# Kernel optimization log

Measured on AMD Instinct MI355X. Metric: run time of the kernel, lower is better.

Reference implementation:

```python
import jax, jax.numpy as jnp
import numpy as np

N = 50000       # num_node
E = 800000      # num edges (avg degree 32)
F_IN, F_HID, F_OUT = 128, 128, 64


def setup_inputs() -> dict:
    key = jax.random.key(0)
    ks = jax.random.split(key, 8)
    x = jax.random.normal(ks[0], (N, F_IN), dtype=jnp.float32)
    edge_index = jax.random.randint(ks[1], (2, E), 0, N, dtype=jnp.int64)
    edge_weight = jax.random.uniform(ks[2], (E,), dtype=jnp.float32)
    s1 = 1.0 / np.sqrt(F_IN)
    s2 = 1.0 / np.sqrt(F_HID)
    W1 = jax.random.normal(ks[3], (F_HID, F_IN), dtype=jnp.float32) * s1
    b1 = jnp.zeros((F_HID,), dtype=jnp.float32)
    W2 = jax.random.normal(ks[4], (F_HID, F_HID), dtype=jnp.float32) * s2
    b2 = jnp.zeros((F_HID,), dtype=jnp.float32)
    W3 = jax.random.normal(ks[5], (F_OUT, F_HID), dtype=jnp.float32) * s2
    b3 = jnp.zeros((F_OUT,), dtype=jnp.float32)
    return {"x": x, "edge_index": edge_index, "edge_weight": edge_weight,
            "W1": W1, "b1": b1, "W2": W2, "b2": b2, "W3": W3, "b3": b3}


def _gcn_norm(edge_index, edge_weight, num_nodes):
    # PyG gcn_norm: add self-loops (weight 1), symmetric D^-1/2 (A+I) D^-1/2
    loop = jnp.arange(num_nodes, dtype=edge_index.dtype)
    row = jnp.concatenate([edge_index[0], loop])  # source
    col = jnp.concatenate([edge_index[1], loop])  # target (aggregation index)
    ew = jnp.concatenate([edge_weight, jnp.ones((num_nodes,), edge_weight.dtype)])
    deg = jax.ops.segment_sum(ew, col, num_segments=num_nodes)
    deg_safe = jnp.where(deg > 0, deg, 1.0)
    dinv = jnp.where(deg > 0, jax.lax.rsqrt(deg_safe), 0.0)
    norm = dinv[row] * ew * dinv[col]  # [E+N]
    return row, col, norm


def reference(x, edge_index, edge_weight, W1, b1, W2, b2, W3, b3):
    num_nodes = x.shape[0]
    row, col, norm = _gcn_norm(edge_index, edge_weight, num_nodes)
    h = x
    for W, b in ((W1, b1), (W2, b2), (W3, b3)):
        m = h @ W.T                                   # [N, d_out]
        msg = m[row] * norm[:, None]                  # gather + scale, [E+N, d_out]
        agg = jax.ops.segment_sum(msg, col, num_segments=num_nodes)
        h = jax.nn.relu(agg + b)                      # GCNConv bias then ReLU
    return h.reshape(-1)                              # torch.flatten
```

## Files before the change

kernel.cpp:

```cpp
#include <hip/hip_runtime.h>
#include <hip/hip_fp16.h>


#define K_DIM 128
#define SORT_ITEMS 4096

typedef unsigned long long u64;
typedef unsigned int u32;

using half8   = __attribute__((ext_vector_type(8))) _Float16;
using floatx4 = __attribute__((ext_vector_type(4))) float;


__global__ void build_hist(const int* __restrict__ row, const int* __restrict__ col,
                           const float* __restrict__ ew, u64* __restrict__ el,
                           u32* __restrict__ ghist, int E, int N, int nb,
                           const float* __restrict__ W1, const float* __restrict__ W2,
                           const float* __restrict__ W3, __half* __restrict__ Wh,
                           int nw1, int nw2, int nw3) {
    const int b = blockIdx.x;
    if (b >= nb) {
        const int i = (b - nb) * 256 + threadIdx.x;
        const int tot = nw1 + nw2 + nw3;
        if (i < tot) {
            float v = (i < nw1) ? W1[i] : (i < nw1 + nw2 ? W2[i - nw1] : W3[i - nw1 - nw2]);
            Wh[i] = __float2half_rn(v);
        }
        return;
    }
    __shared__ u32 bin[256];
    bin[threadIdx.x] = 0;
    __syncthreads();
    const int total = E + N;
    const int base = b * SORT_ITEMS;
    const int end = min(base + SORT_ITEMS, total);
    for (int i = base + threadIdx.x; i < end; i += 256) {
        u64 e;
        if (i < E) {
            e = ((u64)(u32)col[i] << 48) | ((u64)(u32)row[i] << 32)
              | (u64)__float_as_uint(ew[i]);
        } else {
            int v = i - E;
            e = ((u64)(u32)v << 48) | ((u64)(u32)v << 32)
              | (u64)__float_as_uint(1.0f);
        }
        el[i] = e;
        atomicAdd(&bin[(u32)(e >> 56)], 1u);
    }
    __syncthreads();
    ghist[(size_t)threadIdx.x * nb + b] = bin[threadIdx.x];
}

__global__ void digit_sum(const u32* __restrict__ ghist, u32* __restrict__ dsum, int nb) {
    __shared__ u32 s[256];
    const int d = blockIdx.x;
    u32 acc = 0;
    for (int i = threadIdx.x; i < nb; i += 256) acc += ghist[(size_t)d * nb + i];
    s[threadIdx.x] = acc;
    __syncthreads();
    for (int off = 128; off > 0; off >>= 1) {
        if (threadIdx.x < off) s[threadIdx.x] += s[threadIdx.x + off];
        __syncthreads();
    }
    if (threadIdx.x == 0) dsum[d] = s[0];
}

__global__ void digit_scan(u32* __restrict__ ghist, const u32* __restrict__ dsum,
                           u32* __restrict__ dbase, int nb) {
    __shared__ u32 ds[256];
    __shared__ u32 s[256];
    const int d = blockIdx.x, t = threadIdx.x;
    ds[t] = dsum[t];
    __syncthreads();
    for (int off = 1; off < 256; off <<= 1) {
        u32 u = (t >= off) ? ds[t - off] : 0;
        __syncthreads();
        ds[t] += u;
        __syncthreads();
    }
    u32 carry = (d == 0) ? 0u : ds[d - 1];
    if (t == 0) dbase[d] = carry;
    if (d == 255 && t == 0) dbase[256] = ds[255];
    for (int base = 0; base < nb; base += 256) {
        const int i = base + t;
        const u32 v = (i < nb) ? ghist[(size_t)d * nb + i] : 0;
        s[t] = v;
        __syncthreads();
        for (int off = 1; off < 256; off <<= 1) {
            u32 u = (t >= off) ? s[t - off] : 0;
            __syncthreads();
            s[t] += u;
            __syncthreads();
        }
        if (i < nb) ghist[(size_t)d * nb + i] = carry + s[t] - v;
        carry += s[255];
        __syncthreads();
    }
}

__global__ void p1_scatter(const u64* __restrict__ el, const u32* __restrict__ ghist,
                           u64* __restrict__ out, int total, int nb) {
    __shared__ u32 cur[256];
    cur[threadIdx.x] = ghist[(size_t)threadIdx.x * nb + blockIdx.x];
    __syncthreads();
    const int base = blockIdx.x * SORT_ITEMS;
    const int end = min(base + SORT_ITEMS, total);
    for (int i = base + threadIdx.x; i < end; i += 256) {
        u64 e = el[i];
        u32 p = atomicAdd(&cur[(u32)(e >> 56)], 1u);
        out[p] = e;
    }
}

__global__ void p2_sort(const u64* __restrict__ in, u64* __restrict__ out,
                        const u32* __restrict__ dbase,
                        int* __restrict__ offs, float* __restrict__ dinv, int n) {
    const int t = threadIdx.x;
    const int base = (int)dbase[blockIdx.x];
    const int size = (int)dbase[blockIdx.x + 1] - base;
    __shared__ u32 hist[256], cur[256], s[256];
    __shared__ float wsum[256];
    hist[t] = 0;
    wsum[t] = 0.f;
    __syncthreads();
    for (int i = t; i < size; i += 256)
        atomicAdd(&hist[(u32)(in[base + i] >> 48) & 0xFFu], 1u);
    __syncthreads();
    const u32 v = hist[t];
    s[t] = v;
    __syncthreads();
    for (int off = 1; off < 256; off <<= 1) {
        u32 u = (t >= off) ? s[t - off] : 0;
        __syncthreads();
        s[t] += u;
        __syncthreads();
    }
    const u32 mystart = (u32)base + s[t] - v;
    cur[t] = mystart;
    __syncthreads();
    for (int i = t; i < size; i += 256) {
        u64 e = in[base + i];
        u32 lo = (u32)(e >> 48) & 0xFFu;
        u32 p = atomicAdd(&cur[lo], 1u);
        out[p] = e;
        atomicAdd(&wsum[lo], __uint_as_float((u32)(e & 0xFFFFFFFFu)));
    }
    __syncthreads();
    const int node = blockIdx.x * 256 + t;
    if (node < n && v > 0) {
        offs[node] = (int)mystart;
        dinv[node] = rsqrtf(wsum[t]);
        if (node == n - 1) offs[n] = (int)(mystart + v);
    }
}


template <int BN, bool FP32IN>
__global__ __launch_bounds__(256) void mfma_gemm(const void* __restrict__ Ain,
                                                 const __half* __restrict__ Wh,
                                                 const float* __restrict__ dinv,
                                                 __half* __restrict__ C, int nrows) {
    constexpr int NT = BN / 16;
    const int wave = threadIdx.x >> 6;
    const int lane = threadIdx.x & 63;
    const int quad = lane >> 4;
    const int l16  = lane & 15;
    const int row0 = blockIdx.x * 64 + wave * 16;

    int arow = row0 + l16;
    if (arow > nrows - 1) arow = nrows - 1;

    floatx4 acc[NT] = {};

#pragma unroll
    for (int kc = 0; kc < 4; ++kc) {
        const int kof = kc * 32 + quad * 8;
        half8 af;
        if constexpr (FP32IN) {
            const float* ap = (const float*)Ain + (size_t)arow * K_DIM + kof;
            float4 f0 = *(const float4*)ap;
            float4 f1 = *(const float4*)(ap + 4);
            af[0] = (_Float16)f0.x; af[1] = (_Float16)f0.y;
            af[2] = (_Float16)f0.z; af[3] = (_Float16)f0.w;
            af[4] = (_Float16)f1.x; af[5] = (_Float16)f1.y;
            af[6] = (_Float16)f1.z; af[7] = (_Float16)f1.w;
        } else {
            af = *(const half8*)((const __half*)Ain + (size_t)arow * K_DIM + kof);
        }
#pragma unroll
        for (int ct = 0; ct < NT; ++ct) {
            half8 bf = *(const half8*)(Wh + (size_t)(ct * 16 + l16) * K_DIM + kof);
            acc[ct] = __builtin_amdgcn_mfma_f32_16x16x32_f16(af, bf, acc[ct], 0, 0, 0);
        }
    }

    float dv[4];
    int grow[4];
    bool ok[4];
#pragma unroll
    for (int r = 0; r < 4; ++r) {
        grow[r] = row0 + quad * 4 + r;
        ok[r] = grow[r] < nrows;
        dv[r] = ok[r] ? dinv[grow[r]] : 0.f;
    }
#pragma unroll
    for (int ct = 0; ct < NT; ++ct) {
        const int colb = ct * 16 + l16;
#pragma unroll
        for (int r = 0; r < 4; ++r)
            if (ok[r])
                C[(size_t)grow[r] * BN + colb] = __float2half_rn(acc[ct][r] * dv[r]);
    }
}


template <int D, typename OUT>
__global__ __launch_bounds__(256) void agg_kernel(
    const __half* __restrict__ m, const int* __restrict__ offs,
    const int2* __restrict__ csr, const float* __restrict__ dinv,
    const float* __restrict__ bias, OUT* __restrict__ out, int n) {
    const int wid = threadIdx.x >> 6;
    const int lane = threadIdx.x & 63;
    const int node = (blockIdx.x << 2) + wid;
    if (node >= n) return;
    const int beg = offs[node];
    const int end = offs[node + 1];
    const __half2* mh = (const __half2*)m;
    float acc0 = 0.f, acc1 = 0.f;

    if constexpr (D == 128) {
        int k = beg;
        for (; k + 8 <= end; k += 8) {
            int2 e[8];
            float2 f[8];
#pragma unroll
            for (int j = 0; j < 8; ++j) e[j] = csr[k + j];
#pragma unroll
            for (int j = 0; j < 8; ++j)
                f[j] = __half22float2(mh[(size_t)(e[j].y & 0xFFFF) * 64 + lane]);
#pragma unroll
            for (int j = 0; j < 8; ++j) {
                float w = __int_as_float(e[j].x);
                acc0 = fmaf(w, f[j].x, acc0);
                acc1 = fmaf(w, f[j].y, acc1);
            }
        }
        for (; k < end; ++k) {
            int2 e0 = csr[k];
            float w0 = __int_as_float(e0.x);
            float2 f0 = __half22float2(mh[(size_t)(e0.y & 0xFFFF) * 64 + lane]);
            acc0 = fmaf(w0, f0.x, acc0); acc1 = fmaf(w0, f0.y, acc1);
        }
        const float dv = dinv[node];
        const float2 bv = *(const float2*)(bias + 2 * lane);
        float ox = fmaxf(acc0 * dv + bv.x, 0.f);
        float oy = fmaxf(acc1 * dv + bv.y, 0.f);
        if constexpr (sizeof(OUT) == 2) {
            ((__half2*)out)[(size_t)node * 64 + lane] = __floats2half2_rn(ox, oy);
        } else {
            *(float2*)((float*)out + (size_t)node * 128 + 2 * lane) = make_float2(ox, oy);
        }
    } else {
        const int half = lane >> 5;
        const int sl = lane & 31;
        int k = beg;
        for (; k + 8 <= end; k += 8) {
            int2 e0 = csr[k + half], e1 = csr[k + 2 + half];
            int2 e2 = csr[k + 4 + half], e3 = csr[k + 6 + half];
            float2 f0 = __half22float2(mh[(size_t)(e0.y & 0xFFFF) * 32 + sl]);
            float2 f1 = __half22float2(mh[(size_t)(e1.y & 0xFFFF) * 32 + sl]);
            float2 f2 = __half22float2(mh[(size_t)(e2.y & 0xFFFF) * 32 + sl]);
            float2 f3 = __half22float2(mh[(size_t)(e3.y & 0xFFFF) * 32 + sl]);
            float w0 = __int_as_float(e0.x), w1 = __int_as_float(e1.x);
            float w2 = __int_as_float(e2.x), w3 = __int_as_float(e3.x);
            acc0 = fmaf(w0, f0.x, acc0); acc1 = fmaf(w0, f0.y, acc1);
            acc0 = fmaf(w1, f1.x, acc0); acc1 = fmaf(w1, f1.y, acc1);
            acc0 = fmaf(w2, f2.x, acc0); acc1 = fmaf(w2, f2.y, acc1);
            acc0 = fmaf(w3, f3.x, acc0); acc1 = fmaf(w3, f3.y, acc1);
        }
        for (; k + 2 <= end; k += 2) {
            int2 e0 = csr[k + half];
            float w0 = __int_as_float(e0.x);
            float2 f0 = __half22float2(mh[(size_t)(e0.y & 0xFFFF) * 32 + sl]);
            acc0 = fmaf(w0, f0.x, acc0); acc1 = fmaf(w0, f0.y, acc1);
        }
        if (k < end && half == 0) {
            int2 e0 = csr[k];
            float w0 = __int_as_float(e0.x);
            float2 f0 = __half22float2(mh[(size_t)(e0.y & 0xFFFF) * 32 + sl]);
            acc0 = fmaf(w0, f0.x, acc0); acc1 = fmaf(w0, f0.y, acc1);
        }
        acc0 += __shfl_xor(acc0, 32);
        acc1 += __shfl_xor(acc1, 32);
        if (half == 0) {
            const float dv = dinv[node];
            const float2 bv = *(const float2*)(bias + 2 * sl);
            float ox = fmaxf(acc0 * dv + bv.x, 0.f);
            float oy = fmaxf(acc1 * dv + bv.y, 0.f);
            *(float2*)((float*)out + (size_t)node * 64 + 2 * sl) = make_float2(ox, oy);
        }
    }
}


extern "C" void kernel_launch(void* const* d_in, const int* in_sizes, int n_in,
                              void* d_out, int out_size, void* d_ws, size_t ws_size,
                              hipStream_t stream) {
    const float* x  = (const float*)d_in[0];
    const int*   ei = (const int*)d_in[1];
    const float* ew = (const float*)d_in[2];
    const float* W1 = (const float*)d_in[3];
    const float* b1 = (const float*)d_in[4];
    const float* W2 = (const float*)d_in[5];
    const float* b2 = (const float*)d_in[6];
    const float* W3 = (const float*)d_in[7];
    const float* b3 = (const float*)d_in[8];
    float* out = (float*)d_out;

    const int N = in_sizes[0] / K_DIM;
    const int E = in_sizes[2];
    const int* row = ei;
    const int* col = ei + E;

    const int total = E + N;
    const int nb = (total + SORT_ITEMS - 1) / SORT_ITEMS;
    const int ngroups = (N + 255) >> 8;
    const int NW1 = 128 * 128, NW2 = 128 * 128, NW3 = 64 * 128;
    const int nwb = (NW1 + NW2 + NW3 + 255) / 256;

    u64* elA      = (u64*)d_ws;
    u64* elB      = elA + total;
    __half* m_buf = (__half*)(elB + total);
    __half* h_buf = m_buf + (size_t)N * K_DIM;
    __half* Wh    = h_buf + (size_t)N * K_DIM;
    u32* ghist    = (u32*)(Wh + NW1 + NW2 + NW3);
    u32* dsum     = ghist + (size_t)256 * nb;
    u32* dbase    = dsum + 256;
    int* offs     = (int*)(dbase + 257);
    float* dinv   = (float*)(offs + N + 1);

    build_hist<<<nb + nwb, 256, 0, stream>>>(row, col, ew, elA, ghist, E, N, nb,
                                             W1, W2, W3, Wh, NW1, NW2, NW3);
    digit_sum<<<256, 256, 0, stream>>>(ghist, dsum, nb);
    digit_scan<<<256, 256, 0, stream>>>(ghist, dsum, dbase, nb);
    p1_scatter<<<nb, 256, 0, stream>>>(elA, ghist, elB, total, nb);
    p2_sort<<<ngroups, 256, 0, stream>>>(elB, elA, dbase, offs, dinv, N);

    const int gemm_blocks = (N + 63) / 64;
    const int agg_blocks = (N + 3) / 4;
    const int2* csr = (const int2*)elA;

    mfma_gemm<128, true><<<gemm_blocks, 256, 0, stream>>>(x, Wh, dinv, m_buf, N);
    agg_kernel<128, __half><<<agg_blocks, 256, 0, stream>>>(m_buf, offs, csr, dinv, b1, h_buf, N);
    mfma_gemm<128, false><<<gemm_blocks, 256, 0, stream>>>(h_buf, Wh + NW1, dinv, m_buf, N);
    agg_kernel<128, __half><<<agg_blocks, 256, 0, stream>>>(m_buf, offs, csr, dinv, b2, h_buf, N);
    mfma_gemm<64, false><<<gemm_blocks, 256, 0, stream>>>(h_buf, Wh + NW1 + NW2, dinv, m_buf, N);
    agg_kernel<64, float><<<agg_blocks, 256, 0, stream>>>(m_buf, offs, csr, dinv, b3, out, N);
}
```

Baseline: 303.5 us.

## Fuse aggregation with next-layer GEMM and trim sort kernel launches

```diff
diff --git a/kernel.cpp b/kernel.cpp
--- a/kernel.cpp
+++ b/kernel.cpp
@@ -51,26 +51,13 @@
     ghist[(size_t)threadIdx.x * nb + b] = bin[threadIdx.x];
 }
 
-__global__ void digit_sum(const u32* __restrict__ ghist, u32* __restrict__ dsum, int nb) {
-    __shared__ u32 s[256];
-    const int d = blockIdx.x;
-    u32 acc = 0;
-    for (int i = threadIdx.x; i < nb; i += 256) acc += ghist[(size_t)d * nb + i];
-    s[threadIdx.x] = acc;
-    __syncthreads();
-    for (int off = 128; off > 0; off >>= 1) {
-        if (threadIdx.x < off) s[threadIdx.x] += s[threadIdx.x + off];
-        __syncthreads();
-    }
-    if (threadIdx.x == 0) dsum[d] = s[0];
-}
-
-__global__ void digit_scan(u32* __restrict__ ghist, const u32* __restrict__ dsum,
-                           u32* __restrict__ dbase, int nb) {
+__global__ void digit_scan(u32* __restrict__ ghist, u32* __restrict__ dbase, int nb) {
     __shared__ u32 ds[256];
     __shared__ u32 s[256];
     const int d = blockIdx.x, t = threadIdx.x;
-    ds[t] = dsum[t];
+    u32 acc = 0;
+    for (int i = 0; i < nb; ++i) acc += ghist[(size_t)t * nb + i];
+    ds[t] = acc;
     __syncthreads();
     for (int off = 1; off < 256; off <<= 1) {
         u32 u = (t >= off) ? ds[t - off] : 0;
@@ -112,33 +99,36 @@
     }
 }
 
-__global__ void p2_sort(const u64* __restrict__ in, u64* __restrict__ out,
-                        const u32* __restrict__ dbase,
-                        int* __restrict__ offs, float* __restrict__ dinv, int n) {
+__global__ __launch_bounds__(1024) void p2_sort(
+        const u64* __restrict__ in, u64* __restrict__ out,
+        const u32* __restrict__ dbase,
+        int* __restrict__ offs, float* __restrict__ dinv, int n) {
     const int t = threadIdx.x;
     const int base = (int)dbase[blockIdx.x];
     const int size = (int)dbase[blockIdx.x + 1] - base;
     __shared__ u32 hist[256], cur[256], s[256];
     __shared__ float wsum[256];
-    hist[t] = 0;
-    wsum[t] = 0.f;
-    __syncthreads();
-    for (int i = t; i < size; i += 256)
+    if (t < 256) { hist[t] = 0; wsum[t] = 0.f; }
+    __syncthreads();
+    for (int i = t; i < size; i += 1024)
         atomicAdd(&hist[(u32)(in[base + i] >> 48) & 0xFFu], 1u);
     __syncthreads();
-    const u32 v = hist[t];
-    s[t] = v;
+    u32 v = 0;
+    if (t < 256) { v = hist[t]; s[t] = v; }
     __syncthreads();
     for (int off = 1; off < 256; off <<= 1) {
-        u32 u = (t >= off) ? s[t - off] : 0;
-        __syncthreads();
-        s[t] += u;
-        __syncthreads();
-    }
-    const u32 mystart = (u32)base + s[t] - v;
-    cur[t] = mystart;
-    __syncthreads();
-    for (int i = t; i < size; i += 256) {
+        u32 u = (t < 256 && t >= off) ? s[t - off] : 0;
+        __syncthreads();
+        if (t < 256) s[t] += u;
+        __syncthreads();
+    }
+    u32 mystart = 0;
+    if (t < 256) {
+        mystart = (u32)base + s[t] - v;
+        cur[t] = mystart;
+    }
+    __syncthreads();
+    for (int i = t; i < size; i += 1024) {
         u64 e = in[base + i];
         u32 lo = (u32)(e >> 48) & 0xFFu;
         u32 p = atomicAdd(&cur[lo], 1u);
@@ -147,7 +137,7 @@
     }
     __syncthreads();
     const int node = blockIdx.x * 256 + t;
-    if (node < n && v > 0) {
+    if (t < 256 && node < n && v > 0) {
         offs[node] = (int)mystart;
         dinv[node] = rsqrtf(wsum[t]);
         if (node == n - 1) offs[n] = (int)(mystart + v);
@@ -210,6 +200,84 @@
         for (int r = 0; r < 4; ++r)
             if (ok[r])
                 C[(size_t)grow[r] * BN + colb] = __float2half_rn(acc[ct][r] * dv[r]);
+    }
+}
+
+
+template <int BN>
+__global__ __launch_bounds__(256) void fused_agg_gemm(
+    const __half* __restrict__ m, const int* __restrict__ offs,
+    const int2* __restrict__ csr, const float* __restrict__ dinv,
+    const float* __restrict__ bias, const __half* __restrict__ W,
+    __half* __restrict__ out, int n) {
+    const int wid = threadIdx.x >> 6;
+    const int lane = threadIdx.x & 63;
+    const int node0 = blockIdx.x << 2;
+    const int node = node0 + wid;
+    __shared__ __align__(16) __half hs[16][136];
+
+    if (node < n) {
+        const int beg = offs[node];
+        const int end = offs[node + 1];
+        const __half2* mh = (const __half2*)m;
+        float acc0 = 0.f, acc1 = 0.f;
+        int k = beg;
+        for (; k + 8 <= end; k += 8) {
+            int2 e[8];
+            float2 f[8];
+#pragma unroll
+            for (int j = 0; j < 8; ++j) e[j] = csr[k + j];
+#pragma unroll
+            for (int j = 0; j < 8; ++j)
+                f[j] = __half22float2(mh[(size_t)(e[j].y & 0xFFFF) * 64 + lane]);
+#pragma unroll
+            for (int j = 0; j < 8; ++j) {
+                float w = __int_as_float(e[j].x);
+                acc0 = fmaf(w, f[j].x, acc0);
+                acc1 = fmaf(w, f[j].y, acc1);
+            }
+        }
+        for (; k < end; ++k) {
+            int2 e0 = csr[k];
+            float w0 = __int_as_float(e0.x);
+            float2 f0 = __half22float2(mh[(size_t)(e0.y & 0xFFFF) * 64 + lane]);
+            acc0 = fmaf(w0, f0.x, acc0); acc1 = fmaf(w0, f0.y, acc1);
+        }
+        const float dv = dinv[node];
+        const float2 bv = *(const float2*)(bias + 2 * lane);
+        float ox = fmaxf(acc0 * dv + bv.x, 0.f);
+        float oy = fmaxf(acc1 * dv + bv.y, 0.f);
+        ((__half2*)&hs[wid][0])[lane] = __floats2half2_rn(ox, oy);
+    }
+    __syncthreads();
+
+    constexpr int NT = BN / 64;
+    const int quad = lane >> 4;
+    const int l16  = lane & 15;
+    const int colbase = wid * (BN / 4);
+    floatx4 acc[NT] = {};
+#pragma unroll
+    for (int kc = 0; kc < 4; ++kc) {
+        const int kof = kc * 32 + quad * 8;
+        half8 af = *(const half8*)&hs[l16][kof];
+#pragma unroll
+        for (int ct = 0; ct < NT; ++ct) {
+            half8 bf = *(const half8*)(W + (size_t)(colbase + ct * 16 + l16) * K_DIM + kof);
+            acc[ct] = __builtin_amdgcn_mfma_f32_16x16x32_f16(af, bf, acc[ct], 0, 0, 0);
+        }
+    }
+    if (quad == 0) {
+#pragma unroll
+        for (int r = 0; r < 4; ++r) {
+            const int gr = node0 + r;
+            if (gr < n) {
+                const float dv2 = dinv[gr];
+#pragma unroll
+                for (int ct = 0; ct < NT; ++ct)
+                    out[(size_t)gr * BN + colbase + ct * 16 + l16] =
+                        __float2half_rn(acc[ct][r] * dv2);
+            }
+        }
     }
 }
 
@@ -334,26 +402,24 @@
     __half* h_buf = m_buf + (size_t)N * K_DIM;
     __half* Wh    = h_buf + (size_t)N * K_DIM;
     u32* ghist    = (u32*)(Wh + NW1 + NW2 + NW3);
-    u32* dsum     = ghist + (size_t)256 * nb;
-    u32* dbase    = dsum + 256;
+    u32* dbase    = ghist + (size_t)256 * nb;
     int* offs     = (int*)(dbase + 257);
     float* dinv   = (float*)(offs + N + 1);
 
     build_hist<<<nb + nwb, 256, 0, stream>>>(row, col, ew, elA, ghist, E, N, nb,
                                              W1, W2, W3, Wh, NW1, NW2, NW3);
-    digit_sum<<<256, 256, 0, stream>>>(ghist, dsum, nb);
-    digit_scan<<<256, 256, 0, stream>>>(ghist, dsum, dbase, nb);
+    digit_scan<<<256, 256, 0, stream>>>(ghist, dbase, nb);
     p1_scatter<<<nb, 256, 0, stream>>>(elA, ghist, elB, total, nb);
-    p2_sort<<<ngroups, 256, 0, stream>>>(elB, elA, dbase, offs, dinv, N);
+    p2_sort<<<ngroups, 1024, 0, stream>>>(elB, elA, dbase, offs, dinv, N);
 
     const int gemm_blocks = (N + 63) / 64;
     const int agg_blocks = (N + 3) / 4;
     const int2* csr = (const int2*)elA;
 
     mfma_gemm<128, true><<<gemm_blocks, 256, 0, stream>>>(x, Wh, dinv, m_buf, N);
-    agg_kernel<128, __half><<<agg_blocks, 256, 0, stream>>>(m_buf, offs, csr, dinv, b1, h_buf, N);
-    mfma_gemm<128, false><<<gemm_blocks, 256, 0, stream>>>(h_buf, Wh + NW1, dinv, m_buf, N);
-    agg_kernel<128, __half><<<agg_blocks, 256, 0, stream>>>(m_buf, offs, csr, dinv, b2, h_buf, N);
-    mfma_gemm<64, false><<<gemm_blocks, 256, 0, stream>>>(h_buf, Wh + NW1 + NW2, dinv, m_buf, N);
+    fused_agg_gemm<128><<<agg_blocks, 256, 0, stream>>>(m_buf, offs, csr, dinv, b1,
+                                                        Wh + NW1, h_buf, N);
+    fused_agg_gemm<64><<<agg_blocks, 256, 0, stream>>>(h_buf, offs, csr, dinv, b2,
+                                                       Wh + NW1 + NW2, m_buf, N);
     agg_kernel<64, float><<<agg_blocks, 256, 0, stream>>>(m_buf, offs, csr, dinv, b3, out, N);
 }
```

Result: slower. 335.4 us (+10.5%).

## Stage radix scatter through LDS and batch aggregation remainder edges

Applied to the files above, without the earlier changes.

```diff
diff --git a/kernel.cpp b/kernel.cpp
--- a/kernel.cpp
+++ b/kernel.cpp
@@ -98,17 +98,58 @@
     }
 }
 
-__global__ void p1_scatter(const u64* __restrict__ el, const u32* __restrict__ ghist,
-                           u64* __restrict__ out, int total, int nb) {
-    __shared__ u32 cur[256];
-    cur[threadIdx.x] = ghist[(size_t)threadIdx.x * nb + blockIdx.x];
+__global__ __launch_bounds__(256) void p1_scatter(const u64* __restrict__ el,
+                                                  const u32* __restrict__ ghist,
+                                                  u64* __restrict__ out, int total, int nb) {
+    __shared__ u32 gbase[256];
+    __shared__ u32 lbase[256];
+    __shared__ u32 lcur[256];
+    __shared__ u64 buf[SORT_ITEMS];
+    const int t = threadIdx.x;
+    gbase[t] = ghist[(size_t)t * nb + blockIdx.x];
+    lcur[t] = 0;
     __syncthreads();
     const int base = blockIdx.x * SORT_ITEMS;
     const int end = min(base + SORT_ITEMS, total);
-    for (int i = base + threadIdx.x; i < end; i += 256) {
-        u64 e = el[i];
-        u32 p = atomicAdd(&cur[(u32)(e >> 56)], 1u);
-        out[p] = e;
+    const int cnt = end - base;
+
+    u64 it[16];
+    bool ok[16];
+#pragma unroll
+    for (int j = 0; j < 16; ++j) {
+        const int i = base + t + j * 256;
+        ok[j] = i < end;
+        it[j] = ok[j] ? el[i] : 0;
+        if (ok[j]) atomicAdd(&lcur[(u32)(it[j] >> 56)], 1u);
+    }
+    __syncthreads();
+    const u32 v = lcur[t];
+    lbase[t] = v;
+    __syncthreads();
+    for (int off = 1; off < 256; off <<= 1) {
+        u32 u = (t >= off) ? lbase[t - off] : 0;
+        __syncthreads();
+        lbase[t] += u;
+        __syncthreads();
+    }
+    const u32 excl = lbase[t] - v;
+    __syncthreads();
+    lbase[t] = excl;
+    lcur[t] = excl;
+    __syncthreads();
+#pragma unroll
+    for (int j = 0; j < 16; ++j) {
+        if (ok[j]) {
+            const u32 d = (u32)(it[j] >> 56);
+            const u32 p = atomicAdd(&lcur[d], 1u);
+            buf[p] = it[j];
+        }
+    }
+    __syncthreads();
+    for (int i = t; i < cnt; i += 256) {
+        const u64 e = buf[i];
+        const u32 d = (u32)(e >> 56);
+        out[gbase[d] + i - lbase[d]] = e;
     }
 }
 
@@ -225,12 +266,30 @@
     if (node >= n) return;
     const int beg = offs[node];
     const int end = offs[node + 1];
+    const int cnt = end - beg;
+    const int rem = cnt & 7;
     const __half2* mh = (const __half2*)m;
     float acc0 = 0.f, acc1 = 0.f;
 
     if constexpr (D == 128) {
         int k = beg;
-        for (; k + 8 <= end; k += 8) {
+        if (rem) {
+            int2 e[8];
+            float2 f[8];
+#pragma unroll
+            for (int j = 0; j < 8; ++j) e[j] = csr[k + (j < rem ? j : 0)];
+#pragma unroll
+            for (int j = 0; j < 8; ++j)
+                f[j] = __half22float2(mh[(size_t)(e[j].y & 0xFFFF) * 64 + lane]);
+#pragma unroll
+            for (int j = 0; j < 8; ++j) {
+                float w = (j < rem) ? __int_as_float(e[j].x) : 0.f;
+                acc0 = fmaf(w, f[j].x, acc0);
+                acc1 = fmaf(w, f[j].y, acc1);
+            }
+            k += rem;
+        }
+        for (; k < end; k += 8) {
             int2 e[8];
             float2 f[8];
 #pragma unroll
@@ -244,12 +303,6 @@
                 acc0 = fmaf(w, f[j].x, acc0);
                 acc1 = fmaf(w, f[j].y, acc1);
             }
-        }
-        for (; k < end; ++k) {
-            int2 e0 = csr[k];
-            float w0 = __int_as_float(e0.x);
-            float2 f0 = __half22float2(mh[(size_t)(e0.y & 0xFFFF) * 64 + lane]);
-            acc0 = fmaf(w0, f0.x, acc0); acc1 = fmaf(w0, f0.y, acc1);
         }
         const float dv = dinv[node];
         const float2 bv = *(const float2*)(bias + 2 * lane);
@@ -264,7 +317,27 @@
         const int half = lane >> 5;
         const int sl = lane & 31;
         int k = beg;
-        for (; k + 8 <= end; k += 8) {
+        if (rem) {
+            int2 e[4];
+            float2 f[4];
+#pragma unroll
+            for (int jj = 0; jj < 4; ++jj) {
+                const int idx = 2 * jj + half;
+                e[jj] = csr[k + (idx < rem ? idx : 0)];
+            }
+#pragma unroll
+            for (int jj = 0; jj < 4; ++jj)
+                f[jj] = __half22float2(mh[(size_t)(e[jj].y & 0xFFFF) * 32 + sl]);
+#pragma unroll
+            for (int jj = 0; jj < 4; ++jj) {
+                const int idx = 2 * jj + half;
+                float w = (idx < rem) ? __int_as_float(e[jj].x) : 0.f;
+                acc0 = fmaf(w, f[jj].x, acc0);
+                acc1 = fmaf(w, f[jj].y, acc1);
+            }
+            k += rem;
+        }
+        for (; k < end; k += 8) {
             int2 e0 = csr[k + half], e1 = csr[k + 2 + half];
             int2 e2 = csr[k + 4 + half], e3 = csr[k + 6 + half];
             float2 f0 = __half22float2(mh[(size_t)(e0.y & 0xFFFF) * 32 + sl]);
@@ -277,18 +350,6 @@
             acc0 = fmaf(w1, f1.x, acc0); acc1 = fmaf(w1, f1.y, acc1);
             acc0 = fmaf(w2, f2.x, acc0); acc1 = fmaf(w2, f2.y, acc1);
             acc0 = fmaf(w3, f3.x, acc0); acc1 = fmaf(w3, f3.y, acc1);
-        }
-        for (; k + 2 <= end; k += 2) {
-            int2 e0 = csr[k + half];
-            float w0 = __int_as_float(e0.x);
-            float2 f0 = __half22float2(mh[(size_t)(e0.y & 0xFFFF) * 32 + sl]);
-            acc0 = fmaf(w0, f0.x, acc0); acc1 = fmaf(w0, f0.y, acc1);
-        }
-        if (k < end && half == 0) {
-            int2 e0 = csr[k];
-            float w0 = __int_as_float(e0.x);
-            float2 f0 = __half22float2(mh[(size_t)(e0.y & 0xFFFF) * 32 + sl]);
-            acc0 = fmaf(w0, f0.x, acc0); acc1 = fmaf(w0, f0.y, acc1);
         }
         acc0 += __shfl_xor(acc0, 32);
         acc1 += __shfl_xor(acc1, 32);
```

After: 288.3 us. 1.05x faster.
